# Optimization experiments

Hardware: AMD Instinct MI355X
Metric: run time of the kernel (lower is better)

The kernel has to match this reference:

```python
import jax, jax.numpy as jnp
import numpy as np

NUM_HEADS = 4
HEAD_DIM = 32  # out_dim 128 / 4 heads


def setup_inputs() -> dict:
    key = jax.random.key(0)
    ks = jax.random.split(key, 8)
    N, E, R, D = 40000, 640000, 64, 128
    return {
        "entity_emb": jax.random.normal(ks[0], (N, D), jnp.float32),
        "relation_emb": jax.random.normal(ks[1], (R, D), jnp.float32),
        "edge_index": jax.random.randint(ks[2], (2, E), 0, N, jnp.int64),
        "edge_type": jax.random.randint(ks[3], (E,), 0, R, jnp.int64),
        "W": jax.random.normal(ks[4], (D, D), jnp.float32) / np.sqrt(D),
        "W_r": jax.random.normal(ks[5], (D, D), jnp.float32) / np.sqrt(D),
        "attn_w": jax.random.normal(ks[6], (3 * HEAD_DIM, 1), jnp.float32) / np.sqrt(3 * HEAD_DIM),
        "attn_b": jnp.zeros((1,), jnp.float32),
    }


def reference(entity_emb, relation_emb, edge_index, edge_type, W, W_r, attn_w, attn_b):
    N = entity_emb.shape[0]
    H, HD = NUM_HEADS, HEAD_DIM
    # projections (PyTorch Linear: x @ W.T)
    h = (entity_emb @ W.T).reshape(N, H, HD)
    r = relation_emb @ W_r.T
    src, dst = edge_index[0], edge_index[1]
    h_src = h[src]                                    # [E, H, HD]
    h_dst = h[dst]
    r_edge = r[edge_type].reshape(-1, H, HD)
    attn_in = jnp.concatenate([h_src, r_edge, h_dst], axis=-1)  # [E, H, 3*HD]
    scores = jax.nn.leaky_relu(attn_in @ attn_w[:, 0] + attn_b[0], negative_slope=0.2)  # [E, H]
    scores = jnp.exp(scores - jnp.max(scores))
    attn_sum = jax.ops.segment_sum(scores, dst, num_segments=N)  # [N, H]
    attn_weights = scores / (attn_sum[dst] + 1e-8)               # dropout is identity in eval
    msg = attn_weights[..., None] * h_src                        # [E, H, HD]
    out = jax.ops.segment_sum(msg, dst, num_segments=N)          # [N, H, HD]
    return out.reshape(N, H * HD)
```

## Files before the change

### kernel.cpp

```cpp
#include <hip/hip_runtime.h>
#include <math.h>

#define HEADS 4
#define DIM 128
#define LSTRIDE 136

typedef __bf16 bf16x8 __attribute__((ext_vector_type(8)));
typedef float f32x4 __attribute__((ext_vector_type(4)));

__device__ __forceinline__ unsigned short f2bf(float x) {
    unsigned u = __float_as_uint(x);
    unsigned r = (u + 0x7FFFu + ((u >> 16) & 1u)) >> 16;
    return (unsigned short)r;
}
__device__ __forceinline__ float bf2f(unsigned short v) {
    return __uint_as_float(((unsigned)v) << 16);
}

__global__ __launch_bounds__(256) void k_proj(const float* __restrict__ ent,
                                              const float* __restrict__ W,
                                              const float* __restrict__ aw,
                                              const int* __restrict__ ei,
                                              unsigned short* __restrict__ h16,
                                              float4* __restrict__ s1,
                                              float4* __restrict__ s3,
                                              int* __restrict__ deg,
                                              int N, int E) {
    __shared__ unsigned short eL[64 * LSTRIDE];
    __shared__ unsigned short wL[128 * LSTRIDE];
    int t = threadIdx.x;
    int row0 = blockIdx.x * 64;
    const float4* ent4 = (const float4*)ent;
    const float4* W4 = (const float4*)W;
    for (int i = t; i < 64 * 32; i += 256) {
        int r = i >> 5, k4 = i & 31;
        int gr = row0 + r;
        float4 v = (gr < N) ? ent4[(size_t)gr * 32 + k4] : make_float4(0.f, 0.f, 0.f, 0.f);
        unsigned short* p = &eL[r * LSTRIDE + k4 * 4];
        p[0] = f2bf(v.x); p[1] = f2bf(v.y); p[2] = f2bf(v.z); p[3] = f2bf(v.w);
    }
    for (int i = t; i < 128 * 32; i += 256) {
        int r = i >> 5, k4 = i & 31;
        float4 v = W4[r * 32 + k4];
        unsigned short* p = &wL[r * LSTRIDE + k4 * 4];
        p[0] = f2bf(v.x); p[1] = f2bf(v.y); p[2] = f2bf(v.z); p[3] = f2bf(v.w);
    }
    {
        int per = (E + gridDim.x - 1) / gridDim.x;
        int e0 = blockIdx.x * per;
        int e1 = e0 + per;
        if (e1 > E) e1 = E;
        for (int e = e0 + t; e < e1; e += 256) atomicAdd(&deg[ei[E + e]], 1);
    }
    __syncthreads();
    int wv = t >> 6, lane = t & 63, ln = lane & 15, quad = lane >> 4;
    int er = wv * 16 + ln;
    bf16x8 bfr[4];
#pragma unroll
    for (int ks = 0; ks < 4; ++ks)
        bfr[ks] = *(const bf16x8*)&eL[er * LSTRIDE + ks * 32 + quad * 8];
    f32x4 acc[8];
#pragma unroll
    for (int mt = 0; mt < 8; ++mt) acc[mt] = (f32x4){0.f, 0.f, 0.f, 0.f};
#pragma unroll
    for (int ks = 0; ks < 4; ++ks) {
#pragma unroll
        for (int mt = 0; mt < 8; ++mt) {
            bf16x8 afr = *(const bf16x8*)&wL[(mt * 16 + ln) * LSTRIDE + ks * 32 + quad * 8];
            acc[mt] = __builtin_amdgcn_mfma_f32_16x16x32_bf16(afr, bfr[ks], acc[mt], 0, 0, 0);
        }
    }
    int gr = row0 + er;
    const float4* awv = (const float4*)aw;
    float s1h[4] = {0.f, 0.f, 0.f, 0.f}, s3h[4] = {0.f, 0.f, 0.f, 0.f};
#pragma unroll
    for (int mt = 0; mt < 8; ++mt) {
        int d0 = mt * 16 + quad * 4;
        if (gr < N) {
            ushort4 us;
            us.x = f2bf(acc[mt][0]); us.y = f2bf(acc[mt][1]);
            us.z = f2bf(acc[mt][2]); us.w = f2bf(acc[mt][3]);
            *(ushort4*)&h16[(size_t)gr * DIM + d0] = us;
        }
        int wi = (mt & 1) * 4 + quad;
        float4 w1 = awv[wi], w3 = awv[16 + wi];
        int hh = mt >> 1;
        s1h[hh] += acc[mt][0] * w1.x + acc[mt][1] * w1.y + acc[mt][2] * w1.z + acc[mt][3] * w1.w;
        s3h[hh] += acc[mt][0] * w3.x + acc[mt][1] * w3.y + acc[mt][2] * w3.z + acc[mt][3] * w3.w;
    }
#pragma unroll
    for (int hh = 0; hh < HEADS; ++hh) {
        s1h[hh] += __shfl_xor(s1h[hh], 16);
        s1h[hh] += __shfl_xor(s1h[hh], 32);
        s3h[hh] += __shfl_xor(s3h[hh], 16);
        s3h[hh] += __shfl_xor(s3h[hh], 32);
    }
    if (quad == 0 && gr < N) {
        s1[gr] = make_float4(s1h[0], s1h[1], s1h[2], s1h[3]);
        s3[gr] = make_float4(s3h[0], s3h[1], s3h[2], s3h[3]);
    }
}

__global__ __launch_bounds__(256) void k_s2(const float* __restrict__ rel,
                                            const float* __restrict__ Wr,
                                            const float* __restrict__ aw,
                                            float* __restrict__ s2, int RH) {
    __shared__ float v[DIM * HEADS];
    int t = threadIdx.x;
    for (int i = t; i < DIM * HEADS; i += 256) {
        int k = i >> 2, hh = i & 3;
        float a = 0.f;
        for (int j = 0; j < 32; ++j) a += Wr[(hh * 32 + j) * DIM + k] * aw[32 + j];
        v[i] = a;
    }
    __syncthreads();
    int o = blockIdx.x * 4 + (t >> 6);
    if (o >= RH) return;
    int r = o >> 2, hh = o & 3;
    int l = t & 63;
    float p = rel[r * DIM + l] * v[l * 4 + hh] + rel[r * DIM + 64 + l] * v[(64 + l) * 4 + hh];
#pragma unroll
    for (int off = 32; off > 0; off >>= 1) p += __shfl_down(p, off);
    if (l == 0) s2[o] = p;
}

__global__ __launch_bounds__(256) void k_scanA(const int* __restrict__ deg,
                                               int* __restrict__ offs,
                                               int* __restrict__ bsum, int N) {
    __shared__ int sm[256];
    int t = threadIdx.x;
    int i = blockIdx.x * 256 + t;
    int v = (i < N) ? deg[i] : 0;
    sm[t] = v;
    __syncthreads();
    for (int off = 1; off < 256; off <<= 1) {
        int x = (t >= off) ? sm[t - off] : 0;
        __syncthreads();
        sm[t] += x;
        __syncthreads();
    }
    if (i < N) offs[i] = sm[t] - v;
    if (t == 255) bsum[blockIdx.x] = sm[255];
}

__global__ __launch_bounds__(1024) void k_scanB(int* __restrict__ bsum, int nb) {
    __shared__ int partial[1024];
    int t = threadIdx.x;
    int per = (nb + 1023) / 1024;
    int start = t * per;
    int end = start + per;
    if (end > nb) end = nb;
    int sum = 0;
    for (int i = start; i < end; ++i) sum += bsum[i];
    partial[t] = sum;
    __syncthreads();
    for (int off = 1; off < 1024; off <<= 1) {
        int x = (t >= off) ? partial[t - off] : 0;
        __syncthreads();
        partial[t] += x;
        __syncthreads();
    }
    int run = (t > 0) ? partial[t - 1] : 0;
    for (int i = start; i < end; ++i) {
        int v = bsum[i];
        bsum[i] = run;
        run += v;
    }
}

__global__ __launch_bounds__(256) void k_fill(const int* __restrict__ ei,
                                              const int* __restrict__ et,
                                              const int* __restrict__ offs,
                                              const int* __restrict__ bsum,
                                              int* __restrict__ cnt,
                                              int* __restrict__ packed, int E) {
    int e = blockIdx.x * 256 + threadIdx.x;
    if (e >= E) return;
    int dn = ei[E + e];
    int pos = offs[dn] + bsum[dn >> 8] + atomicAdd(&cnt[dn], 1);
    packed[pos] = (ei[e] << 6) | et[e];
}

__global__ __launch_bounds__(64) void k_out(const int* __restrict__ packed,
                                            const int* __restrict__ offs,
                                            const int* __restrict__ bsum,
                                            const float4* __restrict__ s1,
                                            const float4* __restrict__ s2,
                                            const float4* __restrict__ s3,
                                            const float* __restrict__ ab,
                                            const unsigned short* __restrict__ h16,
                                            float* __restrict__ out, int N, int E) {
    __shared__ int src_l[64];
    __shared__ float es_l[64 * 4];
    int n = blockIdx.x;
    int t = threadIdx.x;
    int hh = t >> 4;
    float b = ab[0];
    float4 s3n = s3[n];
    int beg = offs[n] + bsum[n >> 8];
    int end = (n + 1 < N) ? (offs[n + 1] + bsum[(n + 1) >> 8]) : E;
    int cnt = end - beg;
    float a0 = 0.f, a1 = 0.f, sum = 0.f;
    for (int base = 0; base < cnt; base += 64) {
        int m = cnt - base;
        if (m > 64) m = 64;
        __syncthreads();
        if (t < m) {
            int p = packed[beg + base + t];
            int s = p >> 6, ty = p & 63;
            float4 a = s1[s], c = s2[ty];
            float4 sc;
            sc.x = a.x + c.x + s3n.x + b;
            sc.y = a.y + c.y + s3n.y + b;
            sc.z = a.z + c.z + s3n.z + b;
            sc.w = a.w + c.w + s3n.w + b;
            sc.x = sc.x > 0.f ? sc.x : 0.2f * sc.x;
            sc.y = sc.y > 0.f ? sc.y : 0.2f * sc.y;
            sc.z = sc.z > 0.f ? sc.z : 0.2f * sc.z;
            sc.w = sc.w > 0.f ? sc.w : 0.2f * sc.w;
            src_l[t] = s;
            es_l[t * 4 + 0] = __expf(sc.x);
            es_l[t * 4 + 1] = __expf(sc.y);
            es_l[t * 4 + 2] = __expf(sc.z);
            es_l[t * 4 + 3] = __expf(sc.w);
        }
        __syncthreads();
        int i = 0;
        for (; i + 4 <= m; i += 4) {
            int q0 = src_l[i], q1 = src_l[i + 1], q2 = src_l[i + 2], q3 = src_l[i + 3];
            float e0 = es_l[i * 4 + hh], e1 = es_l[(i + 1) * 4 + hh];
            float e2 = es_l[(i + 2) * 4 + hh], e3 = es_l[(i + 3) * 4 + hh];
            unsigned v0 = *(const unsigned*)&h16[(size_t)q0 * DIM + 2 * t];
            unsigned v1 = *(const unsigned*)&h16[(size_t)q1 * DIM + 2 * t];
            unsigned v2 = *(const unsigned*)&h16[(size_t)q2 * DIM + 2 * t];
            unsigned v3 = *(const unsigned*)&h16[(size_t)q3 * DIM + 2 * t];
            sum += (e0 + e1) + (e2 + e3);
            a0 += e0 * bf2f((unsigned short)v0);
            a1 += e0 * bf2f((unsigned short)(v0 >> 16));
            a0 += e1 * bf2f((unsigned short)v1);
            a1 += e1 * bf2f((unsigned short)(v1 >> 16));
            a0 += e2 * bf2f((unsigned short)v2);
            a1 += e2 * bf2f((unsigned short)(v2 >> 16));
            a0 += e3 * bf2f((unsigned short)v3);
            a1 += e3 * bf2f((unsigned short)(v3 >> 16));
        }
        for (; i < m; ++i) {
            int s = src_l[i];
            float e = es_l[i * 4 + hh];
            unsigned v = *(const unsigned*)&h16[(size_t)s * DIM + 2 * t];
            sum += e;
            a0 += e * bf2f((unsigned short)v);
            a1 += e * bf2f((unsigned short)(v >> 16));
        }
    }
    float inv = 1.f / (sum + 1e-8f);
    *(float2*)&out[(size_t)n * DIM + 2 * t] = make_float2(a0 * inv, a1 * inv);
}

extern "C" void kernel_launch(void* const* d_in, const int* in_sizes, int n_in,
                              void* d_out, int out_size, void* d_ws, size_t ws_size,
                              hipStream_t stream) {
    const float* ent = (const float*)d_in[0];
    const float* rel = (const float*)d_in[1];
    const int* ei = (const int*)d_in[2];
    const int* et = (const int*)d_in[3];
    const float* W = (const float*)d_in[4];
    const float* Wr = (const float*)d_in[5];
    const float* aw = (const float*)d_in[6];
    const float* ab = (const float*)d_in[7];

    int N = in_sizes[0] / DIM;
    int R = in_sizes[1] / DIM;
    int E = in_sizes[3];
    int nb = (N + 255) / 256;

    char* w = (char*)d_ws;
    unsigned short* h16 = (unsigned short*)w; w += ((size_t)N * DIM * 2 + 15) / 16 * 16;
    float* s1 = (float*)w;     w += (size_t)N * HEADS * 4;
    float* s3 = (float*)w;     w += (size_t)N * HEADS * 4;
    float* s2 = (float*)w;     w += ((size_t)R * HEADS * 4 + 15) / 16 * 16;
    int* deg = (int*)w;        w += (size_t)N * 4;
    int* cnt = (int*)w;        w += (size_t)N * 4;
    int* offs = (int*)w;       w += ((size_t)N * 4 + 15) / 16 * 16;
    int* bsum = (int*)w;       w += ((size_t)nb * 4 + 15) / 16 * 16;
    int* packed = (int*)w;

    float* out = (float*)d_out;

    (void)hipMemsetAsync(deg, 0, (size_t)N * 8, stream);

    k_proj<<<(N + 63) / 64, 256, 0, stream>>>(ent, W, aw, ei, h16, (float4*)s1,
                                              (float4*)s3, deg, N, E);
    k_s2<<<(R * HEADS + 3) / 4, 256, 0, stream>>>(rel, Wr, aw, s2, R * HEADS);
    k_scanA<<<nb, 256, 0, stream>>>(deg, offs, bsum, N);
    k_scanB<<<1, 1024, 0, stream>>>(bsum, nb);
    k_fill<<<(E + 255) / 256, 256, 0, stream>>>(ei, et, offs, bsum, cnt, packed, E);
    k_out<<<N, 64, 0, stream>>>(packed, offs, bsum, (const float4*)s1, (const float4*)s2,
                                (const float4*)s3, ab, h16, out, N, E);
}
```

Before: 188.6 us.

## Split bf16 conversion and degree count into separate kernel; read operands directly in GEMM

Adds a k_cvt kernel that converts entity embeddings and W to bf16 in workspace and performs the degree atomics, spread over many more blocks. k_proj then drops its LDS staging and barrier and loads MFMA fragments straight from global bf16 buffers. The aim is more parallelism for the conversion and degree count, and lower LDS use so k_proj gets higher occupancy. The costs are an extra launch, an extra global round trip of the bf16 entity matrix, and W fragments re-read from global or L2 by every block.

New measurement: 203.2 us. 7.7% more time.

```diff
diff --git a/kernel.cpp b/kernel.cpp
--- a/kernel.cpp
+++ b/kernel.cpp
@@ -3,7 +3,6 @@
 
 #define HEADS 4
 #define DIM 128
-#define LSTRIDE 136
 
 typedef __bf16 bf16x8 __attribute__((ext_vector_type(8)));
 typedef float f32x4 __attribute__((ext_vector_type(4)));
@@ -17,48 +16,51 @@
     return __uint_as_float(((unsigned)v) << 16);
 }
 
-__global__ __launch_bounds__(256) void k_proj(const float* __restrict__ ent,
-                                              const float* __restrict__ W,
+__global__ __launch_bounds__(256) void k_cvt(const float* __restrict__ ent,
+                                             const float* __restrict__ W,
+                                             const int* __restrict__ ei,
+                                             unsigned short* __restrict__ ent16,
+                                             unsigned short* __restrict__ W16,
+                                             int* __restrict__ deg,
+                                             int N, int E) {
+    int t = threadIdx.x;
+    int i = blockIdx.x * 256 + t;
+    int tot = N * 32;
+    if (i < tot) {
+        float4 v = ((const float4*)ent)[i];
+        ushort4 us;
+        us.x = f2bf(v.x); us.y = f2bf(v.y); us.z = f2bf(v.z); us.w = f2bf(v.w);
+        ((ushort4*)ent16)[i] = us;
+    }
+    if (blockIdx.x < 16) {
+        int j = blockIdx.x * 256 + t;
+        float4 v = ((const float4*)W)[j];
+        ushort4 us;
+        us.x = f2bf(v.x); us.y = f2bf(v.y); us.z = f2bf(v.z); us.w = f2bf(v.w);
+        ((ushort4*)W16)[j] = us;
+    }
+    int per = (E + gridDim.x - 1) / gridDim.x;
+    int e0 = blockIdx.x * per;
+    int e1 = e0 + per;
+    if (e1 > E) e1 = E;
+    for (int e = e0 + t; e < e1; e += 256) atomicAdd(&deg[ei[E + e]], 1);
+}
+
+__global__ __launch_bounds__(256) void k_proj(const unsigned short* __restrict__ ent16,
+                                              const unsigned short* __restrict__ W16,
                                               const float* __restrict__ aw,
-                                              const int* __restrict__ ei,
                                               unsigned short* __restrict__ h16,
                                               float4* __restrict__ s1,
                                               float4* __restrict__ s3,
-                                              int* __restrict__ deg,
-                                              int N, int E) {
-    __shared__ unsigned short eL[64 * LSTRIDE];
-    __shared__ unsigned short wL[128 * LSTRIDE];
-    int t = threadIdx.x;
-    int row0 = blockIdx.x * 64;
-    const float4* ent4 = (const float4*)ent;
-    const float4* W4 = (const float4*)W;
-    for (int i = t; i < 64 * 32; i += 256) {
-        int r = i >> 5, k4 = i & 31;
-        int gr = row0 + r;
-        float4 v = (gr < N) ? ent4[(size_t)gr * 32 + k4] : make_float4(0.f, 0.f, 0.f, 0.f);
-        unsigned short* p = &eL[r * LSTRIDE + k4 * 4];
-        p[0] = f2bf(v.x); p[1] = f2bf(v.y); p[2] = f2bf(v.z); p[3] = f2bf(v.w);
-    }
-    for (int i = t; i < 128 * 32; i += 256) {
-        int r = i >> 5, k4 = i & 31;
-        float4 v = W4[r * 32 + k4];
-        unsigned short* p = &wL[r * LSTRIDE + k4 * 4];
-        p[0] = f2bf(v.x); p[1] = f2bf(v.y); p[2] = f2bf(v.z); p[3] = f2bf(v.w);
-    }
-    {
-        int per = (E + gridDim.x - 1) / gridDim.x;
-        int e0 = blockIdx.x * per;
-        int e1 = e0 + per;
-        if (e1 > E) e1 = E;
-        for (int e = e0 + t; e < e1; e += 256) atomicAdd(&deg[ei[E + e]], 1);
-    }
-    __syncthreads();
+                                              int N) {
+    int t = threadIdx.x;
     int wv = t >> 6, lane = t & 63, ln = lane & 15, quad = lane >> 4;
-    int er = wv * 16 + ln;
+    int er = blockIdx.x * 64 + wv * 16 + ln;
+    int erc = er < N ? er : N - 1;
     bf16x8 bfr[4];
 #pragma unroll
     for (int ks = 0; ks < 4; ++ks)
-        bfr[ks] = *(const bf16x8*)&eL[er * LSTRIDE + ks * 32 + quad * 8];
+        bfr[ks] = *(const bf16x8*)&ent16[(size_t)erc * DIM + ks * 32 + quad * 8];
     f32x4 acc[8];
 #pragma unroll
     for (int mt = 0; mt < 8; ++mt) acc[mt] = (f32x4){0.f, 0.f, 0.f, 0.f};
@@ -66,21 +68,20 @@
     for (int ks = 0; ks < 4; ++ks) {
 #pragma unroll
         for (int mt = 0; mt < 8; ++mt) {
-            bf16x8 afr = *(const bf16x8*)&wL[(mt * 16 + ln) * LSTRIDE + ks * 32 + quad * 8];
+            bf16x8 afr = *(const bf16x8*)&W16[(mt * 16 + ln) * DIM + ks * 32 + quad * 8];
             acc[mt] = __builtin_amdgcn_mfma_f32_16x16x32_bf16(afr, bfr[ks], acc[mt], 0, 0, 0);
         }
     }
-    int gr = row0 + er;
     const float4* awv = (const float4*)aw;
     float s1h[4] = {0.f, 0.f, 0.f, 0.f}, s3h[4] = {0.f, 0.f, 0.f, 0.f};
 #pragma unroll
     for (int mt = 0; mt < 8; ++mt) {
         int d0 = mt * 16 + quad * 4;
-        if (gr < N) {
+        if (er < N) {
             ushort4 us;
             us.x = f2bf(acc[mt][0]); us.y = f2bf(acc[mt][1]);
             us.z = f2bf(acc[mt][2]); us.w = f2bf(acc[mt][3]);
-            *(ushort4*)&h16[(size_t)gr * DIM + d0] = us;
+            *(ushort4*)&h16[(size_t)er * DIM + d0] = us;
         }
         int wi = (mt & 1) * 4 + quad;
         float4 w1 = awv[wi], w3 = awv[16 + wi];
@@ -95,9 +96,9 @@
         s3h[hh] += __shfl_xor(s3h[hh], 16);
         s3h[hh] += __shfl_xor(s3h[hh], 32);
     }
-    if (quad == 0 && gr < N) {
-        s1[gr] = make_float4(s1h[0], s1h[1], s1h[2], s1h[3]);
-        s3[gr] = make_float4(s3h[0], s3h[1], s3h[2], s3h[3]);
+    if (quad == 0 && er < N) {
+        s1[er] = make_float4(s1h[0], s1h[1], s1h[2], s1h[3]);
+        s3[er] = make_float4(s3h[0], s3h[1], s3h[2], s3h[3]);
     }
 }
 
@@ -275,7 +276,9 @@
     int nb = (N + 255) / 256;
 
     char* w = (char*)d_ws;
-    unsigned short* h16 = (unsigned short*)w; w += ((size_t)N * DIM * 2 + 15) / 16 * 16;
+    unsigned short* ent16 = (unsigned short*)w; w += ((size_t)N * DIM * 2 + 15) / 16 * 16;
+    unsigned short* W16 = (unsigned short*)w;   w += (size_t)DIM * DIM * 2;
+    unsigned short* h16 = (unsigned short*)w;   w += ((size_t)N * DIM * 2 + 15) / 16 * 16;
     float* s1 = (float*)w;     w += (size_t)N * HEADS * 4;
     float* s3 = (float*)w;     w += (size_t)N * HEADS * 4;
     float* s2 = (float*)w;     w += ((size_t)R * HEADS * 4 + 15) / 16 * 16;
@@ -289,8 +292,9 @@
 
     (void)hipMemsetAsync(deg, 0, (size_t)N * 8, stream);
 
-    k_proj<<<(N + 63) / 64, 256, 0, stream>>>(ent, W, aw, ei, h16, (float4*)s1,
-                                              (float4*)s3, deg, N, E);
+    k_cvt<<<(N * 32 + 255) / 256, 256, 0, stream>>>(ent, W, ei, ent16, W16, deg, N, E);
+    k_proj<<<(N + 63) / 64, 256, 0, stream>>>(ent16, W16, aw, h16, (float4*)s1,
+                                              (float4*)s3, N);
     k_s2<<<(R * HEADS + 3) / 4, 256, 0, stream>>>(rel, Wr, aw, s2, R * HEADS);
     k_scanA<<<nb, 256, 0, stream>>>(deg, offs, bsum, N);
     k_scanB<<<1, 1024, 0, stream>>>(bsum, nb);
```
